# Kernel optimization log

Hardware: AMD Instinct MI355X
Metric: run time of the kernel (lower is better)

## Reference

```python
import jax, jax.numpy as jnp
import numpy as np

B, T, S, I, H = 64, 64, 512, 512, 512

def setup_inputs() -> dict:
    key = jax.random.key(0)
    ks = jax.random.split(key, 9)
    sc = 0.02
    return {
        "input": jax.random.normal(ks[0], (B, T, I), jnp.float32),
        "h0": jax.random.normal(ks[1], (B, H), jnp.float32),
        "c0": jax.random.normal(ks[2], (B, H), jnp.float32),
        "ctx": jax.random.normal(ks[3], (S, B, H), jnp.float32),
        "W_ih": jax.random.normal(ks[4], (4 * H, I), jnp.float32) * sc,
        "b_ih": jax.random.normal(ks[5], (4 * H,), jnp.float32) * sc,
        "W_hh": jax.random.normal(ks[6], (4 * H, H), jnp.float32) * sc,
        "b_hh": jax.random.normal(ks[7], (4 * H,), jnp.float32) * sc,
        "W_out": jax.random.normal(ks[8], (H, 2 * H), jnp.float32) * sc,
    }

def reference(input, h0, c0, ctx, W_ih, b_ih, W_hh, b_hh, W_out):
    ctx_b = ctx.transpose(1, 0, 2)          # (B, S, H)
    x_tm = input.transpose(1, 0, 2)          # (T, B, I) time-major

    def step(carry, x):
        hx, cx = carry
        gates = x @ W_ih.T + b_ih + hx @ W_hh.T + b_hh   # (B, 4H)
        i, f, g, o = jnp.split(gates, 4, axis=1)          # chunk order: in, forget, cell, out
        ct = jax.nn.sigmoid(f) * cx + jax.nn.sigmoid(i) * jnp.tanh(g)
        ht = jax.nn.sigmoid(o) * jnp.tanh(ct)
        # dot attention over source positions
        scores = jnp.einsum('bsh,bh->bs', ctx_b, ht)      # (B, S)
        attn = jax.nn.softmax(scores, axis=1)
        wc = jnp.einsum('bs,bsh->bh', attn, ctx_b)        # (B, H)
        h_tilde = jnp.tanh(jnp.concatenate([wc, ht], axis=1) @ W_out.T)
        return (ht, ct), h_tilde

    (hT, cT), out = jax.lax.scan(step, (h0, c0), x_tm)    # out: (T, B, H)
    return out.transpose(1, 0, 2), hT, cT
```

## Files before the change

### kernel.cpp

```cpp
#include <hip/hip_runtime.h>
#include <hip/hip_bf16.h>

#define NB 64
#define NT_ 64
#define NS 512
#define NI 512
#define NH 512
#define G4 2048
#define H2 1024
#define BT (NB*NT_)
#define RBLK 64
#define CPB 8

typedef __attribute__((ext_vector_type(8))) short short8;
typedef __attribute__((ext_vector_type(4))) float f32x4;

__device__ __forceinline__ short f2bs(float f) {
    __hip_bfloat16 h = __float2bfloat16(f);
    return *reinterpret_cast<short*>(&h);
}
__device__ __forceinline__ float bs2f(short s) {
    unsigned int u = ((unsigned int)(unsigned short)s) << 16;
    union { unsigned int u; float f; } c; c.u = u; return c.f;
}
__device__ __forceinline__ short8 ld8b(const __hip_bfloat16* p) {
    return *reinterpret_cast<const short8*>(p);
}
__device__ __forceinline__ void ld8f2(const float* p, short8& hi, short8& lo) {
    float4 a = *reinterpret_cast<const float4*>(p);
    float4 b = *reinterpret_cast<const float4*>(p + 4);
    float v[8] = {a.x,a.y,a.z,a.w,b.x,b.y,b.z,b.w};
    #pragma unroll
    for (int i = 0; i < 8; i++) {
        short h = f2bs(v[i]);
        hi[i] = h;
        lo[i] = f2bs(v[i] - bs2f(h));
    }
}
__device__ __forceinline__ float fsigm(float x){ return 1.f/(1.f + __expf(-x)); }
__device__ __forceinline__ float ftanh(float x){ float e = __expf(2.f*x); return 1.f - 2.f/(e + 1.f); }

__global__ __launch_bounds__(256) void conv_split(const float* __restrict__ s,
                                                  __hip_bfloat16* __restrict__ hi,
                                                  __hip_bfloat16* __restrict__ lo, int n) {
    for (int i = blockIdx.x*256 + threadIdx.x; i < n; i += gridDim.x*256) {
        float x = s[i];
        __hip_bfloat16 h = __float2bfloat16(x);
        hi[i] = h;
        lo[i] = __float2bfloat16(x - __bfloat162float(h));
    }
}

__global__ __launch_bounds__(256) void hseq0_init(const float* __restrict__ h0,
                                                  __hip_bfloat16* __restrict__ hs_h,
                                                  __hip_bfloat16* __restrict__ hs_l,
                                                  unsigned* __restrict__ bar) {
    int i = blockIdx.x*256 + threadIdx.x;
    if (i == 0) bar[0] = 0u;
    if (i < NB*NH) {
        float x = h0[i];
        __hip_bfloat16 h = __float2bfloat16(x);
        hs_h[i] = h;
        hs_l[i] = __float2bfloat16(x - __bfloat162float(h));
    }
}

__global__ __launch_bounds__(256) void transpose_ctx(const float* __restrict__ ctx,
                                                     __hip_bfloat16* __restrict__ ctxT) {
    __shared__ float tile[64][65];
    int s0 = blockIdx.x*64, h0 = blockIdx.y*64, b = blockIdx.z;
    int tx = threadIdx.x & 63, ty = threadIdx.x >> 6;
    for (int i = 0; i < 16; i++) {
        int s = i*4 + ty;
        tile[s][tx] = ctx[(size_t)(s0+s)*NB*NH + (size_t)b*NH + h0 + tx];
    }
    __syncthreads();
    for (int i = 0; i < 16; i++) {
        int h = i*4 + ty;
        ctxT[(size_t)b*NH*NS + (size_t)(h0+h)*NS + s0 + tx] = __float2bfloat16(tile[tx][h]);
    }
}

__global__ __launch_bounds__(256) void gemm_xw(const float* __restrict__ X,
                                               const __hip_bfloat16* __restrict__ Wh,
                                               const __hip_bfloat16* __restrict__ Wl,
                                               const float* __restrict__ b_ih,
                                               const float* __restrict__ b_hh,
                                               float* __restrict__ XW) {
    int wid = blockIdx.x*4 + (threadIdx.x>>6);
    int lane = threadIdx.x & 63;
    int m0 = (wid >> 5) * 64;
    int n0 = (wid & 31) * 64;
    int fr = lane & 15, fq = lane >> 4;
    f32x4 acc[4][4] = {};
    for (int kk = 0; kk < NI; kk += 32) {
        short8 ah[4], al[4], bh[4], bl[4];
        #pragma unroll
        for (int i = 0; i < 4; i++) ld8f2(X + (size_t)(m0+i*16+fr)*NI + kk + fq*8, ah[i], al[i]);
        #pragma unroll
        for (int j = 0; j < 4; j++) {
            bh[j] = ld8b(Wh + (size_t)(n0+j*16+fr)*NI + kk + fq*8);
            bl[j] = ld8b(Wl + (size_t)(n0+j*16+fr)*NI + kk + fq*8);
        }
        #pragma unroll
        for (int i = 0; i < 4; i++)
            #pragma unroll
            for (int j = 0; j < 4; j++) {
                acc[i][j] = __builtin_amdgcn_mfma_f32_16x16x32_bf16(ah[i], bh[j], acc[i][j], 0,0,0);
                acc[i][j] = __builtin_amdgcn_mfma_f32_16x16x32_bf16(ah[i], bl[j], acc[i][j], 0,0,0);
                acc[i][j] = __builtin_amdgcn_mfma_f32_16x16x32_bf16(al[i], bh[j], acc[i][j], 0,0,0);
            }
    }
    #pragma unroll
    for (int i = 0; i < 4; i++)
      #pragma unroll
      for (int j = 0; j < 4; j++)
        #pragma unroll
        for (int r = 0; r < 4; r++) {
            int m = m0 + i*16 + fq*4 + r;
            int n = n0 + j*16 + fr;
            XW[(size_t)m*G4 + n] = acc[i][j][r] + b_ih[n] + b_hh[n];
        }
}

__global__ __launch_bounds__(256, 1) void lstm_persist(
    const float* __restrict__ c0,
    const __hip_bfloat16* __restrict__ Whh_h,
    const __hip_bfloat16* __restrict__ Whh_l,
    const float* __restrict__ XW,
    __hip_bfloat16* __restrict__ hs_h,
    __hip_bfloat16* __restrict__ hs_l,
    float* __restrict__ Hf,
    float* __restrict__ hT, float* __restrict__ cT,
    unsigned* __restrict__ bar)
{
    __shared__ __hip_bfloat16 Wh[32*512];
    __shared__ __hip_bfloat16 Wl[32*512];
    __shared__ float gl[64][34];
    int tid = threadIdx.x, bi = blockIdx.x;
    int lane = tid & 63, w = tid >> 6;
    int fr = lane & 15, fq = lane >> 4;

    {
        int jl = tid >> 3, ck8 = tid & 7;
        int grow = (jl >> 3) * NH + bi * CPB + (jl & 7);
        const short8* srcH = (const short8*)(Whh_h + (size_t)grow * NH);
        const short8* srcL = (const short8*)(Whh_l + (size_t)grow * NH);
        #pragma unroll
        for (int cc = 0; cc < 8; cc++) {
            int ck = ck8 * 8 + cc;
            int sw = (ck * 16) ^ ((jl & 7) << 4);
            *(short8*)((char*)Wh + jl * 1024 + sw) = srcH[ck];
            *(short8*)((char*)Wl + jl * 1024 + sw) = srcL[ck];
        }
    }
    int eb  = tid >> 2;
    int ec0 = (tid & 3) * 2;
    float creg[2];
    creg[0] = c0[eb * NH + bi*CPB + ec0];
    creg[1] = c0[eb * NH + bi*CPB + ec0 + 1];
    __syncthreads();

    int m0 = (w & 1) * 32;
    int kh = w >> 1;
    int kbase = kh * 256;

    for (int t = 0; t < NT_; t++) {
        const __hip_bfloat16* Ah = hs_h + (size_t)t * NB * NH;
        const __hip_bfloat16* Al = hs_l + (size_t)t * NB * NH;

        float xwv[2][2][4];
        if (kh == 0) {
            #pragma unroll
            for (int i = 0; i < 2; i++)
              #pragma unroll
              for (int j = 0; j < 2; j++)
                #pragma unroll
                for (int r = 0; r < 4; r++) {
                    int b  = m0 + i*16 + fq*4 + r;
                    int jl = j*16 + fr;
                    xwv[i][j][r] = XW[((size_t)b*NT_ + t)*G4 + (jl>>3)*NH + bi*CPB + (jl&7)];
                }
        }

        f32x4 acc[2][2] = {};
        #pragma unroll
        for (int kk = 0; kk < 256; kk += 32) {
            short8 a_h[2], a_l[2], b_h[2], b_l[2];
            #pragma unroll
            for (int i = 0; i < 2; i++) {
                size_t off = (size_t)(m0 + i*16 + fr) * NH + kbase + kk + fq*8;
                a_h[i] = ld8b(Ah + off);
                a_l[i] = ld8b(Al + off);
            }
            #pragma unroll
            for (int j = 0; j < 2; j++) {
                int jl = j*16 + fr;
                int byt = jl*1024 + ((((kbase + kk + fq*8)*2)) ^ ((jl & 7) << 4));
                b_h[j] = *(const short8*)((const char*)Wh + byt);
                b_l[j] = *(const short8*)((const char*)Wl + byt);
            }
            #pragma unroll
            for (int i = 0; i < 2; i++)
                #pragma unroll
                for (int j = 0; j < 2; j++) {
                    acc[i][j] = __builtin_amdgcn_mfma_f32_16x16x32_bf16(a_h[i], b_h[j], acc[i][j], 0,0,0);
                    acc[i][j] = __builtin_amdgcn_mfma_f32_16x16x32_bf16(a_h[i], b_l[j], acc[i][j], 0,0,0);
                    acc[i][j] = __builtin_amdgcn_mfma_f32_16x16x32_bf16(a_l[i], b_h[j], acc[i][j], 0,0,0);
                }
        }

        if (kh == 0) {
            #pragma unroll
            for (int i = 0; i < 2; i++)
              #pragma unroll
              for (int j = 0; j < 2; j++)
                #pragma unroll
                for (int r = 0; r < 4; r++)
                    gl[m0 + i*16 + fq*4 + r][j*16 + fr] = acc[i][j][r] + xwv[i][j][r];
        }
        __syncthreads();
        if (kh == 1) {
            #pragma unroll
            for (int i = 0; i < 2; i++)
              #pragma unroll
              for (int j = 0; j < 2; j++)
                #pragma unroll
                for (int r = 0; r < 4; r++)
                    gl[m0 + i*16 + fq*4 + r][j*16 + fr] += acc[i][j][r];
        }
        __syncthreads();

        {
            float hv[2];
            #pragma unroll
            for (int u = 0; u < 2; u++) {
                int cl = ec0 + u;
                float gi = gl[eb][cl];
                float gf = gl[eb][8  + cl];
                float gg = gl[eb][16 + cl];
                float go = gl[eb][24 + cl];
                float ct = fsigm(gf)*creg[u] + fsigm(gi)*ftanh(gg);
                hv[u] = fsigm(go)*ftanh(ct);
                creg[u] = ct;
            }
            int hcol = bi*CPB + ec0;
            size_t hoff = (size_t)(t+1)*NB*NH + (size_t)eb*NH + hcol;
            unsigned short h0b = (unsigned short)f2bs(hv[0]);
            unsigned short h1b = (unsigned short)f2bs(hv[1]);
            unsigned ph = (unsigned)h0b | ((unsigned)h1b << 16);
            unsigned short l0b = (unsigned short)f2bs(hv[0] - bs2f((short)h0b));
            unsigned short l1b = (unsigned short)f2bs(hv[1] - bs2f((short)h1b));
            unsigned pl = (unsigned)l0b | ((unsigned)l1b << 16);
            __hip_atomic_store((unsigned*)&hs_h[hoff], ph, __ATOMIC_RELAXED, __HIP_MEMORY_SCOPE_AGENT);
            __hip_atomic_store((unsigned*)&hs_l[hoff], pl, __ATOMIC_RELAXED, __HIP_MEMORY_SCOPE_AGENT);
            *(float2*)&Hf[((size_t)eb*NT_ + t)*NH + hcol] = make_float2(hv[0], hv[1]);
            if (t == NT_-1) {
                *(float2*)&hT[(size_t)eb*NH + hcol] = make_float2(hv[0], hv[1]);
                *(float2*)&cT[(size_t)eb*NH + hcol] = make_float2(creg[0], creg[1]);
            }
        }

        asm volatile("s_waitcnt vmcnt(0)" ::: "memory");
        __syncthreads();
        if (tid == 0) {
            unsigned target = (unsigned)(RBLK * (t+1));
            __hip_atomic_fetch_add(&bar[0], 1u, __ATOMIC_RELAXED, __HIP_MEMORY_SCOPE_AGENT);
            int guard = 0;
            while (__hip_atomic_load(&bar[0], __ATOMIC_RELAXED, __HIP_MEMORY_SCOPE_AGENT) < target) {
                __builtin_amdgcn_s_sleep(2);
                if (++guard > (1<<24)) break;
            }
        }
        __syncthreads();
    }
}

__global__ __launch_bounds__(256) void gemm_scores(const float* __restrict__ Hf,
                                                   const float* __restrict__ ctx,
                                                   float* __restrict__ scores) {
    int wid = blockIdx.x*4 + (threadIdx.x>>6);
    int lane = threadIdx.x & 63;
    int b  = wid >> 3;
    int n0 = (wid & 7) * 64;
    int fr = lane & 15, fq = lane >> 4;
    const float* Ab = Hf + (size_t)b*NT_*NH;
    const float* Bb = ctx + (size_t)b*NH;
    f32x4 acc[4][4] = {};
    for (int kk = 0; kk < NH; kk += 32) {
        short8 ah[4], al[4], bh[4], bl[4];
        #pragma unroll
        for (int i = 0; i < 4; i++) ld8f2(Ab + (size_t)(i*16+fr)*NH + kk + fq*8, ah[i], al[i]);
        #pragma unroll
        for (int j = 0; j < 4; j++) ld8f2(Bb + (size_t)(n0+j*16+fr)*NB*NH + kk + fq*8, bh[j], bl[j]);
        #pragma unroll
        for (int i = 0; i < 4; i++)
            #pragma unroll
            for (int j = 0; j < 4; j++) {
                acc[i][j] = __builtin_amdgcn_mfma_f32_16x16x32_bf16(ah[i], bh[j], acc[i][j], 0,0,0);
                acc[i][j] = __builtin_amdgcn_mfma_f32_16x16x32_bf16(ah[i], bl[j], acc[i][j], 0,0,0);
                acc[i][j] = __builtin_amdgcn_mfma_f32_16x16x32_bf16(al[i], bh[j], acc[i][j], 0,0,0);
            }
    }
    #pragma unroll
    for (int i = 0; i < 4; i++)
      #pragma unroll
      for (int j = 0; j < 4; j++)
        #pragma unroll
        for (int r = 0; r < 4; r++) {
            int t = i*16 + fq*4 + r;
            int s = n0 + j*16 + fr;
            scores[((size_t)b*NT_ + t)*NS + s] = acc[i][j][r];
        }
}

__global__ __launch_bounds__(256) void softmax_rows(const float* __restrict__ scores,
                                                    __hip_bfloat16* __restrict__ ah,
                                                    __hip_bfloat16* __restrict__ al) {
    int row = blockIdx.x*4 + (threadIdx.x>>6);
    int lane = threadIdx.x & 63;
    const float* r = scores + (size_t)row*NS;
    float v[8], mx = -1e30f;
    #pragma unroll
    for (int i = 0; i < 8; i++) { v[i] = r[lane + i*64]; mx = fmaxf(mx, v[i]); }
    #pragma unroll
    for (int off = 32; off; off >>= 1) mx = fmaxf(mx, __shfl_xor(mx, off));
    float sum = 0.f;
    #pragma unroll
    for (int i = 0; i < 8; i++) { v[i] = __expf(v[i]-mx); sum += v[i]; }
    #pragma unroll
    for (int off = 32; off; off >>= 1) sum += __shfl_xor(sum, off);
    float inv = 1.f/sum;
    #pragma unroll
    for (int i = 0; i < 8; i++) {
        float a = v[i]*inv;
        __hip_bfloat16 h = __float2bfloat16(a);
        ah[(size_t)row*NS + lane + i*64] = h;
        al[(size_t)row*NS + lane + i*64] = __float2bfloat16(a - __bfloat162float(h));
    }
}

__global__ __launch_bounds__(256) void gemm_wc(const __hip_bfloat16* __restrict__ Ah,
                                               const __hip_bfloat16* __restrict__ Al,
                                               const __hip_bfloat16* __restrict__ ctxT,
                                               float* __restrict__ Wc) {
    int wid = blockIdx.x*4 + (threadIdx.x>>6);
    int lane = threadIdx.x & 63;
    int b  = wid >> 3;
    int n0 = (wid & 7) * 64;
    int fr = lane & 15, fq = lane >> 4;
    const __hip_bfloat16* Abh = Ah + (size_t)b*NT_*NS;
    const __hip_bfloat16* Abl = Al + (size_t)b*NT_*NS;
    const __hip_bfloat16* Bb  = ctxT + (size_t)b*NH*NS;
    f32x4 acc[4][4] = {};
    for (int kk = 0; kk < NS; kk += 32) {
        short8 ah[4], al[4], bb[4];
        #pragma unroll
        for (int i = 0; i < 4; i++) {
            ah[i] = ld8b(Abh + (size_t)(i*16+fr)*NS + kk + fq*8);
            al[i] = ld8b(Abl + (size_t)(i*16+fr)*NS + kk + fq*8);
        }
        #pragma unroll
        for (int j = 0; j < 4; j++) bb[j] = ld8b(Bb + (size_t)(n0+j*16+fr)*NS + kk + fq*8);
        #pragma unroll
        for (int i = 0; i < 4; i++)
            #pragma unroll
            for (int j = 0; j < 4; j++) {
                acc[i][j] = __builtin_amdgcn_mfma_f32_16x16x32_bf16(ah[i], bb[j], acc[i][j], 0,0,0);
                acc[i][j] = __builtin_amdgcn_mfma_f32_16x16x32_bf16(al[i], bb[j], acc[i][j], 0,0,0);
            }
    }
    #pragma unroll
    for (int i = 0; i < 4; i++)
      #pragma unroll
      for (int j = 0; j < 4; j++)
        #pragma unroll
        for (int r = 0; r < 4; r++) {
            int t = i*16 + fq*4 + r;
            int h = n0 + j*16 + fr;
            Wc[((size_t)b*NT_ + t)*NH + h] = acc[i][j][r];
        }
}

__global__ __launch_bounds__(256) void gemm_out(const float* __restrict__ Wc,
                                                const float* __restrict__ Hf,
                                                const __hip_bfloat16* __restrict__ Wh,
                                                const __hip_bfloat16* __restrict__ Wl,
                                                float* __restrict__ out) {
    int wid = blockIdx.x*4 + (threadIdx.x>>6);
    int lane = threadIdx.x & 63;
    int m0 = (wid >> 3) * 64;
    int n0 = (wid & 7) * 64;
    int fr = lane & 15, fq = lane >> 4;
    f32x4 acc[4][4] = {};
    #pragma unroll 1
    for (int half = 0; half < 2; half++) {
        const float* Am = half ? Hf : Wc;
        int koff = half ? NH : 0;
        for (int kk = 0; kk < NH; kk += 32) {
            short8 ah[4], al[4], bh[4], bl[4];
            #pragma unroll
            for (int i = 0; i < 4; i++) ld8f2(Am + (size_t)(m0+i*16+fr)*NH + kk + fq*8, ah[i], al[i]);
            #pragma unroll
            for (int j = 0; j < 4; j++) {
                bh[j] = ld8b(Wh + (size_t)(n0+j*16+fr)*H2 + koff + kk + fq*8);
                bl[j] = ld8b(Wl + (size_t)(n0+j*16+fr)*H2 + koff + kk + fq*8);
            }
            #pragma unroll
            for (int i = 0; i < 4; i++)
                #pragma unroll
                for (int j = 0; j < 4; j++) {
                    acc[i][j] = __builtin_amdgcn_mfma_f32_16x16x32_bf16(ah[i], bh[j], acc[i][j], 0,0,0);
                    acc[i][j] = __builtin_amdgcn_mfma_f32_16x16x32_bf16(ah[i], bl[j], acc[i][j], 0,0,0);
                    acc[i][j] = __builtin_amdgcn_mfma_f32_16x16x32_bf16(al[i], bh[j], acc[i][j], 0,0,0);
                }
        }
    }
    #pragma unroll
    for (int i = 0; i < 4; i++)
      #pragma unroll
      for (int j = 0; j < 4; j++)
        #pragma unroll
        for (int r = 0; r < 4; r++) {
            int m = m0 + i*16 + fq*4 + r;
            int n = n0 + j*16 + fr;
            out[(size_t)m*NH + n] = ftanh(acc[i][j][r]);
        }
}


extern "C" void kernel_launch(void* const* d_in, const int* in_sizes, int n_in,
                              void* d_out, int out_size, void* d_ws, size_t ws_size,
                              hipStream_t stream) {
    const float* input = (const float*)d_in[0];
    const float* h0    = (const float*)d_in[1];
    const float* c0    = (const float*)d_in[2];
    const float* ctx   = (const float*)d_in[3];
    const float* W_ih  = (const float*)d_in[4];
    const float* b_ih  = (const float*)d_in[5];
    const float* W_hh  = (const float*)d_in[6];
    const float* b_hh  = (const float*)d_in[7];
    const float* W_out = (const float*)d_in[8];
    float* out = (float*)d_out;

    if (ws_size < 94371840u) return;

    char* ws = (char*)d_ws;
    float*          XW     = (float*)(ws + 0);
    float*          scores = (float*)(ws + 0);
    __hip_bfloat16* attn_h = (__hip_bfloat16*)(ws + 8388608);
    __hip_bfloat16* attn_l = (__hip_bfloat16*)(ws + 12582912);
    float*          Hf     = (float*)(ws + 33554432);
    float*          Wc     = (float*)(ws + 41943040);
    __hip_bfloat16* Wih_h  = (__hip_bfloat16*)(ws + 50331648);
    __hip_bfloat16* Wih_l  = (__hip_bfloat16*)(ws + 52428800);
    __hip_bfloat16* Whh_h  = (__hip_bfloat16*)(ws + 54525952);
    __hip_bfloat16* Whh_l  = (__hip_bfloat16*)(ws + 56623104);
    __hip_bfloat16* Wout_h = (__hip_bfloat16*)(ws + 58720256);
    __hip_bfloat16* Wout_l = (__hip_bfloat16*)(ws + 59768832);
    __hip_bfloat16* ctxT   = (__hip_bfloat16*)(ws + 60817408);
    __hip_bfloat16* hs_h   = (__hip_bfloat16*)(ws + 60817408);
    __hip_bfloat16* hs_l   = (__hip_bfloat16*)(ws + 65077248);
    unsigned*       bar    = (unsigned*)(ws + 69337088);

    conv_split<<<2048, 256, 0, stream>>>(W_ih, Wih_h, Wih_l, G4*NI);
    conv_split<<<2048, 256, 0, stream>>>(W_hh, Whh_h, Whh_l, G4*NH);
    conv_split<<<1024, 256, 0, stream>>>(W_out, Wout_h, Wout_l, NH*H2);
    hseq0_init<<<128, 256, 0, stream>>>(h0, hs_h, hs_l, bar);
    gemm_xw<<<512, 256, 0, stream>>>(input, Wih_h, Wih_l, b_ih, b_hh, XW);

    float* hT = out + (size_t)BT*NH;
    float* cT = hT + NB*NH;
    lstm_persist<<<RBLK, 256, 0, stream>>>(c0, Whh_h, Whh_l, XW, hs_h, hs_l, Hf, hT, cT, bar);

    transpose_ctx<<<dim3(8,8,64), 256, 0, stream>>>(ctx, ctxT);
    gemm_scores<<<128, 256, 0, stream>>>(Hf, ctx, scores);
    softmax_rows<<<1024, 256, 0, stream>>>(scores, attn_h, attn_l);
    gemm_wc<<<128, 256, 0, stream>>>(attn_h, attn_l, ctxT, Wc);
    gemm_out<<<128, 256, 0, stream>>>(Wc, Hf, Wout_h, Wout_l, out);
}
```

Baseline: 704.7 us.

## Replace atomic counter barrier with per-block flags and drop fp32 hidden buffer

```diff
diff --git a/kernel.cpp b/kernel.cpp
--- a/kernel.cpp
+++ b/kernel.cpp
@@ -54,9 +54,9 @@
 __global__ __launch_bounds__(256) void hseq0_init(const float* __restrict__ h0,
                                                   __hip_bfloat16* __restrict__ hs_h,
                                                   __hip_bfloat16* __restrict__ hs_l,
-                                                  unsigned* __restrict__ bar) {
+                                                  unsigned* __restrict__ flags) {
     int i = blockIdx.x*256 + threadIdx.x;
-    if (i == 0) bar[0] = 0u;
+    if (i < RBLK*32) flags[i] = 0u;
     if (i < NB*NH) {
         float x = h0[i];
         __hip_bfloat16 h = __float2bfloat16(x);
@@ -130,13 +130,12 @@
     const float* __restrict__ XW,
     __hip_bfloat16* __restrict__ hs_h,
     __hip_bfloat16* __restrict__ hs_l,
-    float* __restrict__ Hf,
     float* __restrict__ hT, float* __restrict__ cT,
-    unsigned* __restrict__ bar)
+    unsigned* __restrict__ flags)
 {
     __shared__ __hip_bfloat16 Wh[32*512];
     __shared__ __hip_bfloat16 Wl[32*512];
-    __shared__ float gl[64][34];
+    __shared__ float gl[4][32][33];
     int tid = threadIdx.x, bi = blockIdx.x;
     int lane = tid & 63, w = tid >> 6;
     int fr = lane & 15, fq = lane >> 4;
@@ -156,32 +155,24 @@
     }
     int eb  = tid >> 2;
     int ec0 = (tid & 3) * 2;
+    int ebl = eb & 31, mhalf = eb >> 5;
     float creg[2];
     creg[0] = c0[eb * NH + bi*CPB + ec0];
     creg[1] = c0[eb * NH + bi*CPB + ec0 + 1];
+    float xw[8];
+    #pragma unroll
+    for (int g = 0; g < 4; g++)
+      #pragma unroll
+      for (int u = 0; u < 2; u++)
+        xw[g*2+u] = XW[(size_t)eb*NT_*G4 + g*NH + bi*CPB + ec0 + u];
     __syncthreads();
 
     int m0 = (w & 1) * 32;
-    int kh = w >> 1;
-    int kbase = kh * 256;
+    int kbase = (w >> 1) * 256;
 
     for (int t = 0; t < NT_; t++) {
         const __hip_bfloat16* Ah = hs_h + (size_t)t * NB * NH;
         const __hip_bfloat16* Al = hs_l + (size_t)t * NB * NH;
-
-        float xwv[2][2][4];
-        if (kh == 0) {
-            #pragma unroll
-            for (int i = 0; i < 2; i++)
-              #pragma unroll
-              for (int j = 0; j < 2; j++)
-                #pragma unroll
-                for (int r = 0; r < 4; r++) {
-                    int b  = m0 + i*16 + fq*4 + r;
-                    int jl = j*16 + fr;
-                    xwv[i][j][r] = XW[((size_t)b*NT_ + t)*G4 + (jl>>3)*NH + bi*CPB + (jl&7)];
-                }
-        }
 
         f32x4 acc[2][2] = {};
         #pragma unroll
@@ -209,74 +200,67 @@
                     acc[i][j] = __builtin_amdgcn_mfma_f32_16x16x32_bf16(a_l[i], b_h[j], acc[i][j], 0,0,0);
                 }
         }
-
-        if (kh == 0) {
-            #pragma unroll
-            for (int i = 0; i < 2; i++)
-              #pragma unroll
-              for (int j = 0; j < 2; j++)
-                #pragma unroll
-                for (int r = 0; r < 4; r++)
-                    gl[m0 + i*16 + fq*4 + r][j*16 + fr] = acc[i][j][r] + xwv[i][j][r];
-        }
+        #pragma unroll
+        for (int i = 0; i < 2; i++)
+          #pragma unroll
+          for (int j = 0; j < 2; j++)
+            #pragma unroll
+            for (int r = 0; r < 4; r++)
+                gl[w][i*16 + fq*4 + r][j*16 + fr] = acc[i][j][r];
         __syncthreads();
-        if (kh == 1) {
-            #pragma unroll
-            for (int i = 0; i < 2; i++)
-              #pragma unroll
-              for (int j = 0; j < 2; j++)
-                #pragma unroll
-                for (int r = 0; r < 4; r++)
-                    gl[m0 + i*16 + fq*4 + r][j*16 + fr] += acc[i][j][r];
-        }
-        __syncthreads();
-
-        {
-            float hv[2];
-            #pragma unroll
-            for (int u = 0; u < 2; u++) {
-                int cl = ec0 + u;
-                float gi = gl[eb][cl];
-                float gf = gl[eb][8  + cl];
-                float gg = gl[eb][16 + cl];
-                float go = gl[eb][24 + cl];
-                float ct = fsigm(gf)*creg[u] + fsigm(gi)*ftanh(gg);
-                hv[u] = fsigm(go)*ftanh(ct);
-                creg[u] = ct;
-            }
-            int hcol = bi*CPB + ec0;
-            size_t hoff = (size_t)(t+1)*NB*NH + (size_t)eb*NH + hcol;
-            unsigned short h0b = (unsigned short)f2bs(hv[0]);
-            unsigned short h1b = (unsigned short)f2bs(hv[1]);
-            unsigned ph = (unsigned)h0b | ((unsigned)h1b << 16);
-            unsigned short l0b = (unsigned short)f2bs(hv[0] - bs2f((short)h0b));
-            unsigned short l1b = (unsigned short)f2bs(hv[1] - bs2f((short)h1b));
-            unsigned pl = (unsigned)l0b | ((unsigned)l1b << 16);
-            __hip_atomic_store((unsigned*)&hs_h[hoff], ph, __ATOMIC_RELAXED, __HIP_MEMORY_SCOPE_AGENT);
-            __hip_atomic_store((unsigned*)&hs_l[hoff], pl, __ATOMIC_RELAXED, __HIP_MEMORY_SCOPE_AGENT);
-            *(float2*)&Hf[((size_t)eb*NT_ + t)*NH + hcol] = make_float2(hv[0], hv[1]);
-            if (t == NT_-1) {
-                *(float2*)&hT[(size_t)eb*NH + hcol] = make_float2(hv[0], hv[1]);
-                *(float2*)&cT[(size_t)eb*NH + hcol] = make_float2(creg[0], creg[1]);
-            }
+
+        float hv[2];
+        #pragma unroll
+        for (int u = 0; u < 2; u++) {
+            int cl = ec0 + u;
+            float gi = gl[mhalf][ebl][cl]      + gl[2+mhalf][ebl][cl]      + xw[u];
+            float gf = gl[mhalf][ebl][8 + cl]  + gl[2+mhalf][ebl][8 + cl]  + xw[2+u];
+            float gg = gl[mhalf][ebl][16 + cl] + gl[2+mhalf][ebl][16 + cl] + xw[4+u];
+            float go = gl[mhalf][ebl][24 + cl] + gl[2+mhalf][ebl][24 + cl] + xw[6+u];
+            float ct = fsigm(gf)*creg[u] + fsigm(gi)*ftanh(gg);
+            hv[u] = fsigm(go)*ftanh(ct);
+            creg[u] = ct;
+        }
+        int hcol = bi*CPB + ec0;
+        size_t hoff = (size_t)(t+1)*NB*NH + (size_t)eb*NH + hcol;
+        unsigned short h0b = (unsigned short)f2bs(hv[0]);
+        unsigned short h1b = (unsigned short)f2bs(hv[1]);
+        unsigned ph = (unsigned)h0b | ((unsigned)h1b << 16);
+        unsigned short l0b = (unsigned short)f2bs(hv[0] - bs2f((short)h0b));
+        unsigned short l1b = (unsigned short)f2bs(hv[1] - bs2f((short)h1b));
+        unsigned pl = (unsigned)l0b | ((unsigned)l1b << 16);
+        __hip_atomic_store((unsigned*)&hs_h[hoff], ph, __ATOMIC_RELAXED, __HIP_MEMORY_SCOPE_AGENT);
+        __hip_atomic_store((unsigned*)&hs_l[hoff], pl, __ATOMIC_RELAXED, __HIP_MEMORY_SCOPE_AGENT);
+        if (t == NT_-1) {
+            *(float2*)&hT[(size_t)eb*NH + hcol] = make_float2(hv[0], hv[1]);
+            *(float2*)&cT[(size_t)eb*NH + hcol] = make_float2(creg[0], creg[1]);
         }
 
         asm volatile("s_waitcnt vmcnt(0)" ::: "memory");
         __syncthreads();
-        if (tid == 0) {
-            unsigned target = (unsigned)(RBLK * (t+1));
-            __hip_atomic_fetch_add(&bar[0], 1u, __ATOMIC_RELAXED, __HIP_MEMORY_SCOPE_AGENT);
+        if (tid == 0)
+            __hip_atomic_store(&flags[bi*32], (unsigned)(t+1), __ATOMIC_RELAXED, __HIP_MEMORY_SCOPE_AGENT);
+        if (t + 1 < NT_) {
+            #pragma unroll
+            for (int g = 0; g < 4; g++)
+              #pragma unroll
+              for (int u = 0; u < 2; u++)
+                xw[g*2+u] = XW[((size_t)eb*NT_ + (t+1))*G4 + g*NH + bi*CPB + ec0 + u];
+        }
+        if (w == 0) {
+            unsigned target = (unsigned)(t+1);
             int guard = 0;
-            while (__hip_atomic_load(&bar[0], __ATOMIC_RELAXED, __HIP_MEMORY_SCOPE_AGENT) < target) {
-                __builtin_amdgcn_s_sleep(2);
-                if (++guard > (1<<24)) break;
+            while (__hip_atomic_load(&flags[lane*32], __ATOMIC_RELAXED, __HIP_MEMORY_SCOPE_AGENT) < target) {
+                __builtin_amdgcn_s_sleep(1);
+                if (++guard > (1<<22)) break;
             }
         }
         __syncthreads();
     }
 }
 
-__global__ __launch_bounds__(256) void gemm_scores(const float* __restrict__ Hf,
+__global__ __launch_bounds__(256) void gemm_scores(const __hip_bfloat16* __restrict__ hs_h,
+                                                   const __hip_bfloat16* __restrict__ hs_l,
                                                    const float* __restrict__ ctx,
                                                    float* __restrict__ scores) {
     int wid = blockIdx.x*4 + (threadIdx.x>>6);
@@ -284,13 +268,18 @@
     int b  = wid >> 3;
     int n0 = (wid & 7) * 64;
     int fr = lane & 15, fq = lane >> 4;
-    const float* Ab = Hf + (size_t)b*NT_*NH;
+    const __hip_bfloat16* Abh = hs_h + NB*NH + (size_t)b*NH;
+    const __hip_bfloat16* Abl = hs_l + NB*NH + (size_t)b*NH;
     const float* Bb = ctx + (size_t)b*NH;
     f32x4 acc[4][4] = {};
     for (int kk = 0; kk < NH; kk += 32) {
         short8 ah[4], al[4], bh[4], bl[4];
         #pragma unroll
-        for (int i = 0; i < 4; i++) ld8f2(Ab + (size_t)(i*16+fr)*NH + kk + fq*8, ah[i], al[i]);
+        for (int i = 0; i < 4; i++) {
+            size_t off = (size_t)(i*16+fr)*NB*NH + kk + fq*8;
+            ah[i] = ld8b(Abh + off);
+            al[i] = ld8b(Abl + off);
+        }
         #pragma unroll
         for (int j = 0; j < 4; j++) ld8f2(Bb + (size_t)(n0+j*16+fr)*NB*NH + kk + fq*8, bh[j], bl[j]);
         #pragma unroll
@@ -383,7 +372,8 @@
 }
 
 __global__ __launch_bounds__(256) void gemm_out(const float* __restrict__ Wc,
-                                                const float* __restrict__ Hf,
+                                                const __hip_bfloat16* __restrict__ hs_h,
+                                                const __hip_bfloat16* __restrict__ hs_l,
                                                 const __hip_bfloat16* __restrict__ Wh,
                                                 const __hip_bfloat16* __restrict__ Wl,
                                                 float* __restrict__ out) {
@@ -393,18 +383,39 @@
     int n0 = (wid & 7) * 64;
     int fr = lane & 15, fq = lane >> 4;
     f32x4 acc[4][4] = {};
-    #pragma unroll 1
-    for (int half = 0; half < 2; half++) {
-        const float* Am = half ? Hf : Wc;
-        int koff = half ? NH : 0;
+    for (int kk = 0; kk < NH; kk += 32) {
+        short8 ah[4], al[4], bh[4], bl[4];
+        #pragma unroll
+        for (int i = 0; i < 4; i++) ld8f2(Wc + (size_t)(m0+i*16+fr)*NH + kk + fq*8, ah[i], al[i]);
+        #pragma unroll
+        for (int j = 0; j < 4; j++) {
+            bh[j] = ld8b(Wh + (size_t)(n0+j*16+fr)*H2 + kk + fq*8);
+            bl[j] = ld8b(Wl + (size_t)(n0+j*16+fr)*H2 + kk + fq*8);
+        }
+        #pragma unroll
+        for (int i = 0; i < 4; i++)
+            #pragma unroll
+            for (int j = 0; j < 4; j++) {
+                acc[i][j] = __builtin_amdgcn_mfma_f32_16x16x32_bf16(ah[i], bh[j], acc[i][j], 0,0,0);
+                acc[i][j] = __builtin_amdgcn_mfma_f32_16x16x32_bf16(ah[i], bl[j], acc[i][j], 0,0,0);
+                acc[i][j] = __builtin_amdgcn_mfma_f32_16x16x32_bf16(al[i], bh[j], acc[i][j], 0,0,0);
+            }
+    }
+    {
+        const __hip_bfloat16* A2h = hs_h + NB*NH + (size_t)(m0>>6)*NH;
+        const __hip_bfloat16* A2l = hs_l + NB*NH + (size_t)(m0>>6)*NH;
         for (int kk = 0; kk < NH; kk += 32) {
             short8 ah[4], al[4], bh[4], bl[4];
             #pragma unroll
-            for (int i = 0; i < 4; i++) ld8f2(Am + (size_t)(m0+i*16+fr)*NH + kk + fq*8, ah[i], al[i]);
+            for (int i = 0; i < 4; i++) {
+                size_t off = (size_t)(i*16+fr)*NB*NH + kk + fq*8;
+                ah[i] = ld8b(A2h + off);
+                al[i] = ld8b(A2l + off);
+            }
             #pragma unroll
             for (int j = 0; j < 4; j++) {
-                bh[j] = ld8b(Wh + (size_t)(n0+j*16+fr)*H2 + koff + kk + fq*8);
-                bl[j] = ld8b(Wl + (size_t)(n0+j*16+fr)*H2 + koff + kk + fq*8);
+                bh[j] = ld8b(Wh + (size_t)(n0+j*16+fr)*H2 + NH + kk + fq*8);
+                bl[j] = ld8b(Wl + (size_t)(n0+j*16+fr)*H2 + NH + kk + fq*8);
             }
             #pragma unroll
             for (int i = 0; i < 4; i++)
@@ -443,39 +454,53 @@
     const float* W_out = (const float*)d_in[8];
     float* out = (float*)d_out;
 
-    if (ws_size < 94371840u) return;
+    const size_t OFF_XW     = 0;
+    const size_t OFF_SCORES = 0;
+    const size_t OFF_ATTN_H = 8388608;
+    const size_t OFF_ATTN_L = 12582912;
+    const size_t OFF_HS_H   = 33554432;
+    const size_t OFF_HS_L   = 37814272;
+    const size_t OFF_FLAGS  = 42074112;
+    const size_t OFF_WC     = 42082304;
+    const size_t OFF_WIH_H  = 50470912;
+    const size_t OFF_WIH_L  = 52568064;
+    const size_t OFF_WHH_H  = 54665216;
+    const size_t OFF_WHH_L  = 56762368;
+    const size_t OFF_WOUT_H = 58859520;
+    const size_t OFF_WOUT_L = 59908096;
+    const size_t OFF_CTXT   = 60956672;
+    if (ws_size < 94511104u) return;
 
     char* ws = (char*)d_ws;
-    float*          XW     = (float*)(ws + 0);
-    float*          scores = (float*)(ws + 0);
-    __hip_bfloat16* attn_h = (__hip_bfloat16*)(ws + 8388608);
-    __hip_bfloat16* attn_l = (__hip_bfloat16*)(ws + 12582912);
-    float*          Hf     = (float*)(ws + 33554432);
-    float*          Wc     = (float*)(ws + 41943040);
-    __hip_bfloat16* Wih_h  = (__hip_bfloat16*)(ws + 50331648);
-    __hip_bfloat16* Wih_l  = (__hip_bfloat16*)(ws + 52428800);
-    __hip_bfloat16* Whh_h  = (__hip_bfloat16*)(ws + 54525952);
-    __hip_bfloat16* Whh_l  = (__hip_bfloat16*)(ws + 56623104);
-    __hip_bfloat16* Wout_h = (__hip_bfloat16*)(ws + 58720256);
-    __hip_bfloat16* Wout_l = (__hip_bfloat16*)(ws + 59768832);
-    __hip_bfloat16* ctxT   = (__hip_bfloat16*)(ws + 60817408);
-    __hip_bfloat16* hs_h   = (__hip_bfloat16*)(ws + 60817408);
-    __hip_bfloat16* hs_l   = (__hip_bfloat16*)(ws + 65077248);
-    unsigned*       bar    = (unsigned*)(ws + 69337088);
+    float*          XW     = (float*)(ws + OFF_XW);
+    float*          scores = (float*)(ws + OFF_SCORES);
+    __hip_bfloat16* attn_h = (__hip_bfloat16*)(ws + OFF_ATTN_H);
+    __hip_bfloat16* attn_l = (__hip_bfloat16*)(ws + OFF_ATTN_L);
+    __hip_bfloat16* hs_h   = (__hip_bfloat16*)(ws + OFF_HS_H);
+    __hip_bfloat16* hs_l   = (__hip_bfloat16*)(ws + OFF_HS_L);
+    unsigned*       flags  = (unsigned*)(ws + OFF_FLAGS);
+    float*          Wc     = (float*)(ws + OFF_WC);
+    __hip_bfloat16* Wih_h  = (__hip_bfloat16*)(ws + OFF_WIH_H);
+    __hip_bfloat16* Wih_l  = (__hip_bfloat16*)(ws + OFF_WIH_L);
+    __hip_bfloat16* Whh_h  = (__hip_bfloat16*)(ws + OFF_WHH_H);
+    __hip_bfloat16* Whh_l  = (__hip_bfloat16*)(ws + OFF_WHH_L);
+    __hip_bfloat16* Wout_h = (__hip_bfloat16*)(ws + OFF_WOUT_H);
+    __hip_bfloat16* Wout_l = (__hip_bfloat16*)(ws + OFF_WOUT_L);
+    __hip_bfloat16* ctxT   = (__hip_bfloat16*)(ws + OFF_CTXT);
 
     conv_split<<<2048, 256, 0, stream>>>(W_ih, Wih_h, Wih_l, G4*NI);
     conv_split<<<2048, 256, 0, stream>>>(W_hh, Whh_h, Whh_l, G4*NH);
     conv_split<<<1024, 256, 0, stream>>>(W_out, Wout_h, Wout_l, NH*H2);
-    hseq0_init<<<128, 256, 0, stream>>>(h0, hs_h, hs_l, bar);
+    hseq0_init<<<128, 256, 0, stream>>>(h0, hs_h, hs_l, flags);
     gemm_xw<<<512, 256, 0, stream>>>(input, Wih_h, Wih_l, b_ih, b_hh, XW);
 
     float* hT = out + (size_t)BT*NH;
     float* cT = hT + NB*NH;
-    lstm_persist<<<RBLK, 256, 0, stream>>>(c0, Whh_h, Whh_l, XW, hs_h, hs_l, Hf, hT, cT, bar);
+    lstm_persist<<<RBLK, 256, 0, stream>>>(c0, Whh_h, Whh_l, XW, hs_h, hs_l, hT, cT, flags);
 
     transpose_ctx<<<dim3(8,8,64), 256, 0, stream>>>(ctx, ctxT);
-    gemm_scores<<<128, 256, 0, stream>>>(Hf, ctx, scores);
+    gemm_scores<<<128, 256, 0, stream>>>(hs_h, hs_l, ctx, scores);
     softmax_rows<<<1024, 256, 0, stream>>>(scores, attn_h, attn_l);
     gemm_wc<<<128, 256, 0, stream>>>(attn_h, attn_l, ctxT, Wc);
-    gemm_out<<<128, 256, 0, stream>>>(Wc, Hf, Wout_h, Wout_l, out);
-}
+    gemm_out<<<128, 256, 0, stream>>>(Wc, hs_h, hs_l, Wout_h, Wout_l, out);
+}
```

After: 658.3 us. -6.6%, faster.
